# Optimization experiments

Hardware: AMD Instinct MI355X
Metric: run time of the kernel (lower is better)

## Reference

```python
import jax, jax.numpy as jnp
import numpy as np

STRIDE = 2
P = 2


def setup_inputs() -> dict:
    key = jax.random.key(0)
    x = jax.random.normal(key, (32, 256, 64, 64), dtype=jnp.float32)
    return {"x": x}


def reference(x) -> jnp.ndarray:
    s = STRIDE
    b, c, h, w = x.shape
    # circular pad on the right/bottom if spatial dims are odd
    pad_h = h % 2
    pad_w = w % 2
    if pad_h or pad_w:
        x = jnp.pad(x, ((0, 0), (0, 0), (0, pad_h), (0, pad_w)), mode="wrap")
    h2, w2 = x.shape[2] // s, x.shape[3] // s
    # all s*s polyphase components: comps[i*s+j] == x[:, :, i::s, j::s]
    comps = x.reshape(b, c, h2, s, w2, s)
    comps = comps.transpose(3, 5, 0, 1, 2, 4).reshape(s * s, b, c, h2, w2)
    # p-norm per (component, batch) over channels + spatial dims
    norms = jnp.sum(jnp.abs(comps) ** P, axis=(2, 3, 4)) ** (1.0 / P)  # [s*s, b]
    max_idx = jnp.argmax(norms, axis=0)  # [b]
    selected = comps[max_idx, jnp.arange(b)]  # [b, c, h2, w2]
    return selected
```

## Files before the change

### kernel.cpp

```cpp
#include <hip/hip_runtime.h>


#define B 32
#define C 256
#define H 64
#define W 64
#define H2 32
#define W2 32
#define NBLK 64
#define IN_F4_PER_BATCH (C * H * W / 4)
#define T1 (NBLK * 256)
#define ITER1 (IN_F4_PER_BATCH / T1)
#define SEL_F2_PER_BATCH (C * H2 * W2 / 2)
#define GBLK 128
#define T2 (GBLK * 256)
#define ITER2 (SEL_F2_PER_BATCH / T2)

typedef float floatx2 __attribute__((ext_vector_type(2)));

__global__ __launch_bounds__(256, 8) void aps_partials(const float4* __restrict__ x,
                                                       float* __restrict__ ws) {
    const int b = blockIdx.y;
    const float4* xb = x + (size_t)b * IN_F4_PER_BATCH;
    const int q0 = blockIdx.x * 256 + threadIdx.x;
    float sA = 0.f, sB = 0.f;
#pragma unroll 4
    for (int it = 0; it < ITER1; ++it) {
        float4 v = xb[q0 + it * T1];
        sA += v.x * v.x + v.z * v.z;
        sB += v.y * v.y + v.w * v.w;
    }
    sA += __shfl_down(sA, 32);  sB += __shfl_down(sB, 32);
#pragma unroll
    for (int off = 8; off; off >>= 1) {
        sA += __shfl_down(sA, off);  sB += __shfl_down(sB, off);
    }
    __shared__ float sm[4][4];
    const int lane = threadIdx.x & 63;
    const int wave = threadIdx.x >> 6;
    if (lane == 0)  { sm[wave][0] = sA; sm[wave][1] = sB; }
    if (lane == 16) { sm[wave][2] = sA; sm[wave][3] = sB; }
    __syncthreads();
    if (threadIdx.x < 4) {
        const int k = threadIdx.x;
        float t = sm[0][k] + sm[1][k] + sm[2][k] + sm[3][k];
        ws[(b * 4 + k) * NBLK + blockIdx.x] = t;
    }
}

__global__ __launch_bounds__(256, 8) void aps_gather(const float4* __restrict__ x,
                                                     const float* __restrict__ ws,
                                                     floatx2* __restrict__ out) {
    const int b = blockIdx.y;
    const int lane = threadIdx.x & 63;
    const int wave = threadIdx.x >> 6;
    float p = ws[(b * 4 + wave) * NBLK + lane];
    for (int off = 32; off; off >>= 1) p += __shfl_down(p, off);
    __shared__ float s4[4];
    if (lane == 0) s4[wave] = p;
    __syncthreads();
    const float v0 = s4[0], v1 = s4[1], v2 = s4[2], v3 = s4[3];
    float best = v0;
    int k = 0;
    if (v1 > best) { best = v1; k = 1; }
    if (v2 > best) { best = v2; k = 2; }
    if (v3 > best) { k = 3; }
    const int di = k >> 1;
    const int dj = k & 1;

    const float4* xb = x + (size_t)b * IN_F4_PER_BATCH;
    floatx2* ob = out + (size_t)b * SEL_F2_PER_BATCH;
    const int m0 = blockIdx.x * 256 + threadIdx.x;
#pragma unroll
    for (int it = 0; it < ITER2; ++it) {
        const int m   = m0 + it * T2;
        const int ch  = m >> 9;
        const int r   = (m >> 4) & 31;
        const int col = m & 15;
        float4 v = xb[(ch * 64 + 2 * r + di) * 16 + col];
        floatx2 o;
        if (dj == 0) { o.x = v.x; o.y = v.z; }
        else         { o.x = v.y; o.y = v.w; }
        __builtin_nontemporal_store(o, ob + m);
    }
}

extern "C" void kernel_launch(void* const* d_in, const int* in_sizes, int n_in,
                              void* d_out, int out_size, void* d_ws, size_t ws_size,
                              hipStream_t stream) {
    const float* x = (const float*)d_in[0];
    float* out = (float*)d_out;
    float* ws = (float*)d_ws;

    aps_partials<<<dim3(NBLK, B), 256, 0, stream>>>((const float4*)x, ws);
    aps_gather<<<dim3(GBLK, B), 256, 0, stream>>>((const float4*)x, ws, (floatx2*)out);
}
```

Before: 209.1 us.

## Fuse partial-norm and gather kernels via cooperative grid sync

Merges the norm-partials and gather kernels into one cooperative kernel that computes per-block partial sums, performs a grid-wide sync, then selects the argmax component and gathers its slice. It keeps the two-kernel path as a fallback if cooperative launch fails. This removes a kernel launch boundary and may let gather reads hit cache, at the cost of a grid barrier and the requirement that all blocks be co-resident. The partials loop unroll is also raised.

After: 780.0 us. 3.73x slower.

```diff
diff --git a/kernel.cpp b/kernel.cpp
--- a/kernel.cpp
+++ b/kernel.cpp
@@ -1,4 +1,7 @@
 #include <hip/hip_runtime.h>
+#include <hip/hip_cooperative_groups.h>
+
+namespace cg = cooperative_groups;
 
 
 #define B 32
@@ -12,19 +15,20 @@
 #define T1 (NBLK * 256)
 #define ITER1 (IN_F4_PER_BATCH / T1)
 #define SEL_F2_PER_BATCH (C * H2 * W2 / 2)
+#define F2_PER_BLK (SEL_F2_PER_BATCH / NBLK)
+#define ITER2 (F2_PER_BLK / 256)
 #define GBLK 128
 #define T2 (GBLK * 256)
-#define ITER2 (SEL_F2_PER_BATCH / T2)
+#define ITER2F (SEL_F2_PER_BATCH / T2)
 
 typedef float floatx2 __attribute__((ext_vector_type(2)));
 
-__global__ __launch_bounds__(256, 8) void aps_partials(const float4* __restrict__ x,
-                                                       float* __restrict__ ws) {
-    const int b = blockIdx.y;
-    const float4* xb = x + (size_t)b * IN_F4_PER_BATCH;
-    const int q0 = blockIdx.x * 256 + threadIdx.x;
+__device__ __forceinline__ void partials_phase(const float4* __restrict__ xb,
+                                               float* __restrict__ ws,
+                                               int b, int bx) {
+    const int q0 = bx * 256 + threadIdx.x;
     float sA = 0.f, sB = 0.f;
-#pragma unroll 4
+#pragma unroll 8
     for (int it = 0; it < ITER1; ++it) {
         float4 v = xb[q0 + it * T1];
         sA += v.x * v.x + v.z * v.z;
@@ -44,14 +48,11 @@
     if (threadIdx.x < 4) {
         const int k = threadIdx.x;
         float t = sm[0][k] + sm[1][k] + sm[2][k] + sm[3][k];
-        ws[(b * 4 + k) * NBLK + blockIdx.x] = t;
+        ws[(b * 4 + k) * NBLK + bx] = t;
     }
 }
 
-__global__ __launch_bounds__(256, 8) void aps_gather(const float4* __restrict__ x,
-                                                     const float* __restrict__ ws,
-                                                     floatx2* __restrict__ out) {
-    const int b = blockIdx.y;
+__device__ __forceinline__ int argmax_phase(const float* __restrict__ ws, int b) {
     const int lane = threadIdx.x & 63;
     const int wave = threadIdx.x >> 6;
     float p = ws[(b * 4 + wave) * NBLK + lane];
@@ -65,33 +66,79 @@
     if (v1 > best) { best = v1; k = 1; }
     if (v2 > best) { best = v2; k = 2; }
     if (v3 > best) { k = 3; }
+    return k;
+}
+
+__device__ __forceinline__ void gather_m(const float4* __restrict__ xb,
+                                         floatx2* __restrict__ ob,
+                                         int m, int di, int dj) {
+    const int ch  = m >> 9;
+    const int r   = (m >> 4) & 31;
+    const int col = m & 15;
+    float4 v = xb[(ch * 64 + 2 * r + di) * 16 + col];
+    floatx2 o;
+    if (dj == 0) { o.x = v.x; o.y = v.z; }
+    else         { o.x = v.y; o.y = v.w; }
+    __builtin_nontemporal_store(o, ob + m);
+}
+
+__global__ __launch_bounds__(256, 8) void aps_fused(const float4* __restrict__ x,
+                                                    float* __restrict__ ws,
+                                                    floatx2* __restrict__ out) {
+    const int b  = blockIdx.y;
+    const int bx = blockIdx.x;
+    const float4* xb = x + (size_t)b * IN_F4_PER_BATCH;
+
+    partials_phase(xb, ws, b, bx);
+
+    __threadfence();
+    cg::this_grid().sync();
+    __threadfence();
+
+    const int k  = argmax_phase(ws, b);
     const int di = k >> 1;
     const int dj = k & 1;
 
+    floatx2* ob = out + (size_t)b * SEL_F2_PER_BATCH;
+    const int m0 = bx * F2_PER_BLK + threadIdx.x;
+#pragma unroll
+    for (int it = 0; it < ITER2; ++it)
+        gather_m(xb, ob, m0 + it * 256, di, dj);
+}
+
+__global__ __launch_bounds__(256, 8) void aps_partials(const float4* __restrict__ x,
+                                                       float* __restrict__ ws) {
+    const int b = blockIdx.y;
+    partials_phase(x + (size_t)b * IN_F4_PER_BATCH, ws, b, blockIdx.x);
+}
+
+__global__ __launch_bounds__(256, 8) void aps_gather(const float4* __restrict__ x,
+                                                     const float* __restrict__ ws,
+                                                     floatx2* __restrict__ out) {
+    const int b  = blockIdx.y;
+    const int k  = argmax_phase(ws, b);
+    const int di = k >> 1, dj = k & 1;
     const float4* xb = x + (size_t)b * IN_F4_PER_BATCH;
     floatx2* ob = out + (size_t)b * SEL_F2_PER_BATCH;
     const int m0 = blockIdx.x * 256 + threadIdx.x;
 #pragma unroll
-    for (int it = 0; it < ITER2; ++it) {
-        const int m   = m0 + it * T2;
-        const int ch  = m >> 9;
-        const int r   = (m >> 4) & 31;
-        const int col = m & 15;
-        float4 v = xb[(ch * 64 + 2 * r + di) * 16 + col];
-        floatx2 o;
-        if (dj == 0) { o.x = v.x; o.y = v.z; }
-        else         { o.x = v.y; o.y = v.w; }
-        __builtin_nontemporal_store(o, ob + m);
-    }
+    for (int it = 0; it < ITER2F; ++it)
+        gather_m(xb, ob, m0 + it * T2, di, dj);
 }
 
 extern "C" void kernel_launch(void* const* d_in, const int* in_sizes, int n_in,
                               void* d_out, int out_size, void* d_ws, size_t ws_size,
                               hipStream_t stream) {
-    const float* x = (const float*)d_in[0];
-    float* out = (float*)d_out;
+    const float4* x = (const float4*)d_in[0];
     float* ws = (float*)d_ws;
+    floatx2* out = (floatx2*)d_out;
 
-    aps_partials<<<dim3(NBLK, B), 256, 0, stream>>>((const float4*)x, ws);
-    aps_gather<<<dim3(GBLK, B), 256, 0, stream>>>((const float4*)x, ws, (floatx2*)out);
+    void* args[] = {(void*)&x, (void*)&ws, (void*)&out};
+    hipError_t e = hipLaunchCooperativeKernel((const void*)aps_fused,
+                                              dim3(NBLK, B), dim3(256),
+                                              args, 0, stream);
+    if (e != hipSuccess) {
+        aps_partials<<<dim3(NBLK, B), 256, 0, stream>>>(x, ws);
+        aps_gather<<<dim3(GBLK, B), 256, 0, stream>>>(x, ws, out);
+    }
 }
```

## Fuse norm reduction and gather into one kernel with per-batch spin barrier

Applied to the files above, without the earlier changes.

Merges the partial-norm kernel and the gather kernel into a single launch. Blocks of the same batch publish their partial sums and then spin on an atomic counter until all 64 blocks have arrived. Each block now reduces and gathers the same contiguous four-channel slice, so the gather re-read is more likely to hit cache, and the second launch goes away. The cost is a memset launch, spin-wait time, and reliance on all blocks of a batch being co-resident. A guard bounds the spin, but if it ever expires the kernel could silently pick the wrong component.

After: 390.4 us. +86.7%, slower.

```diff
diff --git a/kernel.cpp b/kernel.cpp
--- a/kernel.cpp
+++ b/kernel.cpp
@@ -5,28 +5,32 @@
 #define C 256
 #define H 64
 #define W 64
-#define H2 32
-#define W2 32
 #define NBLK 64
 #define IN_F4_PER_BATCH (C * H * W / 4)
-#define T1 (NBLK * 256)
-#define ITER1 (IN_F4_PER_BATCH / T1)
-#define SEL_F2_PER_BATCH (C * H2 * W2 / 2)
-#define GBLK 128
-#define T2 (GBLK * 256)
-#define ITER2 (SEL_F2_PER_BATCH / T2)
+#define F4_PER_BLK (IN_F4_PER_BATCH / NBLK)
+#define ITER1 (F4_PER_BLK / 256)
+#define SEL_F2_PER_BATCH (C * 32 * 32 / 2)
+#define F2_PER_BLK (SEL_F2_PER_BATCH / NBLK)
+#define ITER2 (F2_PER_BLK / 256)
+#define SPIN_GUARD (1 << 19)
 
 typedef float floatx2 __attribute__((ext_vector_type(2)));
 
-__global__ __launch_bounds__(256, 8) void aps_partials(const float4* __restrict__ x,
-                                                       float* __restrict__ ws) {
-    const int b = blockIdx.y;
+__global__ __launch_bounds__(256, 8) void aps_fused(const float4* __restrict__ x,
+                                                    unsigned* __restrict__ cnt,
+                                                    float* __restrict__ part,
+                                                    floatx2* __restrict__ out) {
+    const int b  = blockIdx.y;
+    const int bx = blockIdx.x;
     const float4* xb = x + (size_t)b * IN_F4_PER_BATCH;
-    const int q0 = blockIdx.x * 256 + threadIdx.x;
+    const int lane = threadIdx.x & 63;
+    const int wave = threadIdx.x >> 6;
+
+    const int q0 = bx * F4_PER_BLK + threadIdx.x;
     float sA = 0.f, sB = 0.f;
-#pragma unroll 4
+#pragma unroll 8
     for (int it = 0; it < ITER1; ++it) {
-        float4 v = xb[q0 + it * T1];
+        float4 v = xb[q0 + it * 256];
         sA += v.x * v.x + v.z * v.z;
         sB += v.y * v.y + v.w * v.w;
     }
@@ -36,25 +40,32 @@
         sA += __shfl_down(sA, off);  sB += __shfl_down(sB, off);
     }
     __shared__ float sm[4][4];
-    const int lane = threadIdx.x & 63;
-    const int wave = threadIdx.x >> 6;
     if (lane == 0)  { sm[wave][0] = sA; sm[wave][1] = sB; }
     if (lane == 16) { sm[wave][2] = sA; sm[wave][3] = sB; }
     __syncthreads();
     if (threadIdx.x < 4) {
         const int k = threadIdx.x;
         float t = sm[0][k] + sm[1][k] + sm[2][k] + sm[3][k];
-        ws[(b * 4 + k) * NBLK + blockIdx.x] = t;
+        __hip_atomic_store(&part[(b * 4 + k) * NBLK + bx], t,
+                           __ATOMIC_RELAXED, __HIP_MEMORY_SCOPE_AGENT);
     }
-}
+    __syncthreads();
 
-__global__ __launch_bounds__(256, 8) void aps_gather(const float4* __restrict__ x,
-                                                     const float* __restrict__ ws,
-                                                     floatx2* __restrict__ out) {
-    const int b = blockIdx.y;
-    const int lane = threadIdx.x & 63;
-    const int wave = threadIdx.x >> 6;
-    float p = ws[(b * 4 + wave) * NBLK + lane];
+    if (threadIdx.x == 0) {
+        __hip_atomic_fetch_add(&cnt[b], 1u,
+                               __ATOMIC_RELEASE, __HIP_MEMORY_SCOPE_AGENT);
+        int guard = 0;
+        while (__hip_atomic_load(&cnt[b], __ATOMIC_RELAXED,
+                                 __HIP_MEMORY_SCOPE_AGENT) < NBLK &&
+               guard < SPIN_GUARD) {
+            __builtin_amdgcn_s_sleep(8);
+            ++guard;
+        }
+    }
+    __syncthreads();
+
+    float p = __hip_atomic_load(&part[(b * 4 + wave) * NBLK + lane],
+                                __ATOMIC_RELAXED, __HIP_MEMORY_SCOPE_AGENT);
     for (int off = 32; off; off >>= 1) p += __shfl_down(p, off);
     __shared__ float s4[4];
     if (lane == 0) s4[wave] = p;
@@ -68,12 +79,11 @@
     const int di = k >> 1;
     const int dj = k & 1;
 
-    const float4* xb = x + (size_t)b * IN_F4_PER_BATCH;
     floatx2* ob = out + (size_t)b * SEL_F2_PER_BATCH;
-    const int m0 = blockIdx.x * 256 + threadIdx.x;
+    const int m0 = bx * F2_PER_BLK + threadIdx.x;
 #pragma unroll
     for (int it = 0; it < ITER2; ++it) {
-        const int m   = m0 + it * T2;
+        const int m   = m0 + it * 256;
         const int ch  = m >> 9;
         const int r   = (m >> 4) & 31;
         const int col = m & 15;
@@ -88,10 +98,11 @@
 extern "C" void kernel_launch(void* const* d_in, const int* in_sizes, int n_in,
                               void* d_out, int out_size, void* d_ws, size_t ws_size,
                               hipStream_t stream) {
-    const float* x = (const float*)d_in[0];
-    float* out = (float*)d_out;
-    float* ws = (float*)d_ws;
+    const float4* x = (const float4*)d_in[0];
+    unsigned* cnt = (unsigned*)d_ws;
+    float* part = (float*)d_ws + 64;
+    floatx2* out = (floatx2*)d_out;
 
-    aps_partials<<<dim3(NBLK, B), 256, 0, stream>>>((const float4*)x, ws);
-    aps_gather<<<dim3(GBLK, B), 256, 0, stream>>>((const float4*)x, ws, (floatx2*)out);
+    hipMemsetAsync(d_ws, 0, 128, stream);
+    aps_fused<<<dim3(NBLK, B), 256, 0, stream>>>(x, cnt, part, out);
 }
```
